# Optimization experiments

Hardware: AMD Instinct MI355X
Metric: run time of the kernel (lower is better)

## Reference

```python
import jax, jax.numpy as jnp
import numpy as np

NUM_USERS = 100000
NUM_ITEMS = 100000
EMB = 64
BATCH = 8192
TEMP = 0.2  # config['temperature']


def _l2norm(x):
    # F.normalize(x, dim=-1): x / max(||x||_2, eps)
    return x / jnp.maximum(jnp.linalg.norm(x, axis=-1, keepdims=True), 1e-12)


def setup_inputs() -> dict:
    key = jax.random.key(0)
    k1, k2, k3, k4, k5 = jax.random.split(key, 5)
    # xavier_uniform bounds for the embedding tables
    bu = float(np.sqrt(6.0 / (NUM_USERS + EMB)))
    bi = float(np.sqrt(6.0 / (NUM_ITEMS + EMB)))
    return {
        "user": jax.random.randint(k1, (BATCH,), 0, NUM_USERS),
        "positive": jax.random.randint(k2, (BATCH,), 0, NUM_ITEMS),
        "negative": jax.random.randint(k3, (BATCH,), 0, NUM_ITEMS),
        "user_emb_weight": jax.random.uniform(k4, (NUM_USERS, EMB), jnp.float32, -bu, bu),
        "item_emb_weight": jax.random.uniform(k5, (NUM_ITEMS, EMB), jnp.float32, -bi, bi),
    }


def reference(user, positive, negative, user_emb_weight, item_emb_weight):
    # encoder == 'MF': raw embedding tables are used directly.
    u = _l2norm(user_emb_weight[user])        # [B, D]
    p = _l2norm(item_emb_weight[positive])    # [B, D]

    # positive ('up') term: per-pair inner products
    ip = jnp.sum(u * p, axis=1)               # [B]
    up = jnp.mean(jnp.log(jnp.exp(ip / TEMP) + jnp.exp(ip * ip / TEMP)))

    # 'down' term. Original computes score over unique(user) x unique(positive)
    # weighted by the outer product of occurrence counts, then takes mean.
    # sum_{unique u,i} c_u*c_i*f(sim(u,i)) == sum over all BxB batch pairs of
    # f(sim(user_b, pos_b')), so we use the full batch cross product (jit-safe)
    # and divide by (#unique users * #unique items) for the mean.
    sim = u @ p.T                              # [B, B]
    score_sum = jnp.sum(jnp.exp(sim / TEMP) + jnp.exp(sim * sim / TEMP))
    nu = jnp.sum(jnp.bincount(user, length=NUM_USERS) > 0).astype(sim.dtype)
    ni = jnp.sum(jnp.bincount(positive, length=NUM_ITEMS) > 0).astype(sim.dtype)
    down = jnp.log(score_sum / (nu * ni))

    # loss_list = [-up, down]
    return jnp.stack([-up, down])
```

## Files before the change

kernel.cpp:

```cpp
#include <hip/hip_runtime.h>
#include <hip/hip_bf16.h>

#define EMB 64

typedef __attribute__((ext_vector_type(8))) short short8;
typedef __attribute__((ext_vector_type(8))) __bf16 bf16x8;
typedef __attribute__((ext_vector_type(4))) float f32x4;

__device__ inline f32x4 mfma16x16x32(short8 a, short8 b, f32x4 c) {
  return __builtin_amdgcn_mfma_f32_16x16x32_bf16(
      __builtin_bit_cast(bf16x8, a), __builtin_bit_cast(bf16x8, b), c, 0, 0, 0);
}

#define EXP2_HW __builtin_amdgcn_exp2f
#define C5LOG2E 7.213475204444817f

__global__ __launch_bounds__(256) void clear_kernel(uint4* __restrict__ p) {
  const int i = blockIdx.x * 256 + threadIdx.x;
  if (i < 12500) p[i] = make_uint4(0u, 0u, 0u, 0u);
}

__global__ __launch_bounds__(256) void prep_kernel(
    const int* __restrict__ user, const int* __restrict__ pos,
    const float* __restrict__ uw, const float* __restrict__ iw,
    __hip_bfloat16* __restrict__ u_bf, __hip_bfloat16* __restrict__ p_bf,
    unsigned char* __restrict__ uflag, unsigned char* __restrict__ iflag,
    float* __restrict__ up_p)
{
  const int tid  = threadIdx.x;
  const int wave = tid >> 6;
  const int lane = tid & 63;
  const int e    = lane & 15;
  const int row  = blockIdx.x * 16 + wave * 4 + (lane >> 4);

  const int uidx = user[row];
  const int pidx = pos[row];
  const float4 uv = *reinterpret_cast<const float4*>(&uw[(size_t)uidx * EMB + e * 4]);
  const float4 pv = *reinterpret_cast<const float4*>(&iw[(size_t)pidx * EMB + e * 4]);

  float us = uv.x*uv.x + uv.y*uv.y + uv.z*uv.z + uv.w*uv.w;
  float ps = pv.x*pv.x + pv.y*pv.y + pv.z*pv.z + pv.w*pv.w;
  #pragma unroll
  for (int off = 1; off < 16; off <<= 1) {
    us += __shfl_xor(us, off);
    ps += __shfl_xor(ps, off);
  }
  const float ur = 1.0f / fmaxf(sqrtf(us), 1e-12f);
  const float pr = 1.0f / fmaxf(sqrtf(ps), 1e-12f);
  const float4 un = make_float4(uv.x*ur, uv.y*ur, uv.z*ur, uv.w*ur);
  const float4 pn = make_float4(pv.x*pr, pv.y*pr, pv.z*pr, pv.w*pr);

  ushort4 ub, pb;
  ub.x = __bfloat16_as_ushort(__float2bfloat16(un.x));
  ub.y = __bfloat16_as_ushort(__float2bfloat16(un.y));
  ub.z = __bfloat16_as_ushort(__float2bfloat16(un.z));
  ub.w = __bfloat16_as_ushort(__float2bfloat16(un.w));
  pb.x = __bfloat16_as_ushort(__float2bfloat16(pn.x));
  pb.y = __bfloat16_as_ushort(__float2bfloat16(pn.y));
  pb.z = __bfloat16_as_ushort(__float2bfloat16(pn.z));
  pb.w = __bfloat16_as_ushort(__float2bfloat16(pn.w));
  *reinterpret_cast<ushort4*>(&u_bf[(size_t)row * EMB + e * 4]) = ub;
  *reinterpret_cast<ushort4*>(&p_bf[(size_t)row * EMB + e * 4]) = pb;

  float ip = un.x*pn.x + un.y*pn.y + un.z*pn.z + un.w*pn.w;
  #pragma unroll
  for (int off = 1; off < 16; off <<= 1) ip += __shfl_xor(ip, off);

  float upv = 0.0f;
  if (e == 0) {
    uflag[uidx] = 1;
    iflag[pidx] = 1;
    const float t = ip * C5LOG2E;
    upv = logf(EXP2_HW(t) + EXP2_HW(ip * t));
  }
  upv += __shfl_xor(upv, 16);
  upv += __shfl_xor(upv, 32);

  __shared__ float sred[4];
  if (lane == 0) sred[wave] = upv;
  __syncthreads();
  if (tid == 0)
    up_p[blockIdx.x] = (sred[0] + sred[1]) + (sred[2] + sred[3]);
}

__global__ __launch_bounds__(256) void gemm_kernel(
    const __hip_bfloat16* __restrict__ U, const __hip_bfloat16* __restrict__ P,
    float* __restrict__ dn_p)
{
  const int by  = blockIdx.x >> 4;
  const int bx0 = (blockIdx.x & 15) << 2;
  const int wave = threadIdx.x >> 6;
  const int lane = threadIdx.x & 63;
  const int r0 = by * 128 + (wave >> 1) * 64;
  const int lrow = lane & 15;
  const int lk   = (lane >> 4) * 8;

  short8 a[4][2];
  #pragma unroll
  for (int i = 0; i < 4; ++i)
    #pragma unroll
    for (int kk = 0; kk < 2; ++kk)
      a[i][kk] = *reinterpret_cast<const short8*>(
          &U[(size_t)(r0 + i * 16 + lrow) * EMB + kk * 32 + lk]);

  float s0 = 0.0f, s1 = 0.0f, s2 = 0.0f, s3 = 0.0f;

  auto loadB = [&](int t, int h, short8 (&b)[2][2]) {
    const int c0 = (bx0 + t) * 128 + (wave & 1) * 64 + h * 32;
    #pragma unroll
    for (int j = 0; j < 2; ++j)
      #pragma unroll
      for (int kk = 0; kk < 2; ++kk)
        b[j][kk] = *reinterpret_cast<const short8*>(
            &P[(size_t)(c0 + j * 16 + lrow) * EMB + kk * 32 + lk]);
  };
  auto procHalf = [&](const short8 (&b)[2][2]) {
    f32x4 acc[4][2] = {};
    #pragma unroll
    for (int i = 0; i < 4; ++i)
      #pragma unroll
      for (int j = 0; j < 2; ++j) {
        acc[i][j] = mfma16x16x32(a[i][0], b[j][0], acc[i][j]);
        acc[i][j] = mfma16x16x32(a[i][1], b[j][1], acc[i][j]);
      }
    #pragma unroll
    for (int i = 0; i < 4; ++i)
      #pragma unroll
      for (int j = 0; j < 2; ++j)
        #pragma unroll
        for (int r = 0; r < 4; ++r) {
          const float v  = acc[i][j][r];
          const float tt = v * C5LOG2E;
          if (j) { s2 += EXP2_HW(tt); s3 += EXP2_HW(v * tt); }
          else   { s0 += EXP2_HW(tt); s1 += EXP2_HW(v * tt); }
        }
  };

  short8 bA[2][2], bB[2][2];
  loadB(0, 0, bA);
  #pragma unroll 1
  for (int t = 0; t < 4; ++t) {
    loadB(t, 1, bB);
    procHalf(bA);
    loadB((t + 1) & 3, 0, bA);
    procHalf(bB);
  }

  float s = (s0 + s1) + (s2 + s3);
  #pragma unroll
  for (int off = 32; off; off >>= 1) s += __shfl_xor(s, off);

  __shared__ float sred[4];
  if (lane == 0) sred[wave] = s;
  __syncthreads();
  if (threadIdx.x == 0)
    dn_p[blockIdx.x] = (sred[0] + sred[1]) + (sred[2] + sred[3]);
}

__global__ __launch_bounds__(1024) void finalize_kernel(
    const float* __restrict__ up_p, const float* __restrict__ dn_p,
    const uint4* __restrict__ uflag4, const uint4* __restrict__ iflag4,
    float* __restrict__ out)
{
  const int tid  = threadIdx.x;
  const int wave = tid >> 6;
  const int lane = tid & 63;

  float upv = (tid < 512) ? up_p[tid] : 0.0f;
  float dnv = dn_p[tid];
  int uc = 0, ic = 0;
  for (int i = tid; i < 6250; i += 1024) {
    uint4 v = uflag4[i];
    uc += __popc(v.x) + __popc(v.y) + __popc(v.z) + __popc(v.w);
    uint4 w = iflag4[i];
    ic += __popc(w.x) + __popc(w.y) + __popc(w.z) + __popc(w.w);
  }

  #pragma unroll
  for (int off = 32; off; off >>= 1) {
    upv += __shfl_xor(upv, off);
    dnv += __shfl_xor(dnv, off);
    uc  += __shfl_xor(uc, off);
    ic  += __shfl_xor(ic, off);
  }

  __shared__ float sf[2][16];
  __shared__ int   si[2][16];
  if (lane == 0) { sf[0][wave] = upv; sf[1][wave] = dnv; si[0][wave] = uc; si[1][wave] = ic; }
  __syncthreads();
  if (tid == 0) {
    float usum = 0.0f, dsum = 0.0f; int nu = 0, ni = 0;
    #pragma unroll
    for (int w = 0; w < 16; ++w) {
      usum += sf[0][w]; dsum += sf[1][w]; nu += si[0][w]; ni += si[1][w];
    }
    out[0] = -(usum / 8192.0f);
    out[1] = logf(dsum / ((float)nu * (float)ni));
  }
}

extern "C" void kernel_launch(void* const* d_in, const int* in_sizes, int n_in,
                              void* d_out, int out_size, void* d_ws, size_t ws_size,
                              hipStream_t stream) {
  const int*   user = (const int*)d_in[0];
  const int*   pos  = (const int*)d_in[1];
  const float* uw   = (const float*)d_in[3];
  const float* iw   = (const float*)d_in[4];
  float* out = (float*)d_out;

  char* ws = (char*)d_ws;
  __hip_bfloat16* u_bf = (__hip_bfloat16*)(ws);
  __hip_bfloat16* p_bf = (__hip_bfloat16*)(ws + (1u << 20));
  uint4* flag4 = (uint4*)(ws + (2u << 20));
  unsigned char* uflag = (unsigned char*)flag4;
  unsigned char* iflag = uflag + 100000;
  float* up_p = (float*)(ws + (2u << 20) + 200704);
  float* dn_p = up_p + 512;

  clear_kernel<<<49, 256, 0, stream>>>(flag4);
  prep_kernel<<<512, 256, 0, stream>>>(user, pos, uw, iw, u_bf, p_bf,
                                       uflag, iflag, up_p);
  gemm_kernel<<<1024, 256, 0, stream>>>(u_bf, p_bf, dn_p);
  finalize_kernel<<<1, 1024, 0, stream>>>(up_p, dn_p,
                                          (const uint4*)uflag,
                                          (const uint4*)iflag, out);
}
```

Baseline: 42.56 us.

## Fuse finalize into GEMM via last-block counter and LDS bitmap unique count

Removes the clear kernel and the finalize kernel. The last GEMM block to finish, found through an atomic counter that prep_kernel resets, builds the unique-user and unique-item bitmaps in shared memory and performs the final reduction. This cuts two kernel launches and the global flag-array traffic. The cost is a 25KB shared bitmap in every GEMM block, which may reduce occupancy, plus the loss of the software double-buffering of B loads.

```diff
diff --git a/kernel.cpp b/kernel.cpp
--- a/kernel.cpp
+++ b/kernel.cpp
@@ -14,24 +14,20 @@
 
 #define EXP2_HW __builtin_amdgcn_exp2f
 #define C5LOG2E 7.213475204444817f
-
-__global__ __launch_bounds__(256) void clear_kernel(uint4* __restrict__ p) {
-  const int i = blockIdx.x * 256 + threadIdx.x;
-  if (i < 12500) p[i] = make_uint4(0u, 0u, 0u, 0u);
-}
 
 __global__ __launch_bounds__(256) void prep_kernel(
     const int* __restrict__ user, const int* __restrict__ pos,
     const float* __restrict__ uw, const float* __restrict__ iw,
     __hip_bfloat16* __restrict__ u_bf, __hip_bfloat16* __restrict__ p_bf,
-    unsigned char* __restrict__ uflag, unsigned char* __restrict__ iflag,
-    float* __restrict__ up_p)
+    float* __restrict__ up_p, unsigned int* __restrict__ done_cnt)
 {
   const int tid  = threadIdx.x;
   const int wave = tid >> 6;
   const int lane = tid & 63;
   const int e    = lane & 15;
   const int row  = blockIdx.x * 16 + wave * 4 + (lane >> 4);
+
+  if (blockIdx.x == 0 && tid == 0) *done_cnt = 0u;
 
   const int uidx = user[row];
   const int pidx = pos[row];
@@ -68,8 +64,6 @@
 
   float upv = 0.0f;
   if (e == 0) {
-    uflag[uidx] = 1;
-    iflag[pidx] = 1;
     const float t = ip * C5LOG2E;
     upv = logf(EXP2_HW(t) + EXP2_HW(ip * t));
   }
@@ -85,15 +79,22 @@
 
 __global__ __launch_bounds__(256) void gemm_kernel(
     const __hip_bfloat16* __restrict__ U, const __hip_bfloat16* __restrict__ P,
-    float* __restrict__ dn_p)
+    const int* __restrict__ user, const int* __restrict__ pos,
+    const float* __restrict__ up_p, float* __restrict__ dn_p,
+    unsigned int* __restrict__ done_cnt, float* __restrict__ out)
 {
-  const int by  = blockIdx.x >> 4;
-  const int bx0 = (blockIdx.x & 15) << 2;
-  const int wave = threadIdx.x >> 6;
-  const int lane = threadIdx.x & 63;
-  const int r0 = by * 128 + (wave >> 1) * 64;
+  const int tid  = threadIdx.x;
+  const int by   = blockIdx.x >> 4;
+  const int bx0  = (blockIdx.x & 15) << 2;
+  const int wave = tid >> 6;
+  const int lane = tid & 63;
+  const int r0   = by * 128 + (wave >> 1) * 64;
   const int lrow = lane & 15;
   const int lk   = (lane >> 4) * 8;
+
+  __shared__ float sredf[4];
+  __shared__ unsigned int bitmap[6250];
+  __shared__ unsigned int is_last;
 
   short8 a[4][2];
   #pragma unroll
@@ -105,16 +106,18 @@
 
   float s0 = 0.0f, s1 = 0.0f, s2 = 0.0f, s3 = 0.0f;
 
-  auto loadB = [&](int t, int h, short8 (&b)[2][2]) {
-    const int c0 = (bx0 + t) * 128 + (wave & 1) * 64 + h * 32;
+  #pragma unroll 1
+  for (int s = 0; s < 8; ++s) {
+    const int c0 = (bx0 + (s >> 1)) * 128 + (wave & 1) * 64 + (s & 1) * 32;
+
+    short8 b[2][2];
     #pragma unroll
     for (int j = 0; j < 2; ++j)
       #pragma unroll
       for (int kk = 0; kk < 2; ++kk)
         b[j][kk] = *reinterpret_cast<const short8*>(
             &P[(size_t)(c0 + j * 16 + lrow) * EMB + kk * 32 + lk]);
-  };
-  auto procHalf = [&](const short8 (&b)[2][2]) {
+
     f32x4 acc[4][2] = {};
     #pragma unroll
     for (int i = 0; i < 4; ++i)
@@ -123,6 +126,7 @@
         acc[i][j] = mfma16x16x32(a[i][0], b[j][0], acc[i][j]);
         acc[i][j] = mfma16x16x32(a[i][1], b[j][1], acc[i][j]);
       }
+
     #pragma unroll
     for (int i = 0; i < 4; ++i)
       #pragma unroll
@@ -134,47 +138,42 @@
           if (j) { s2 += EXP2_HW(tt); s3 += EXP2_HW(v * tt); }
           else   { s0 += EXP2_HW(tt); s1 += EXP2_HW(v * tt); }
         }
-  };
-
-  short8 bA[2][2], bB[2][2];
-  loadB(0, 0, bA);
-  #pragma unroll 1
-  for (int t = 0; t < 4; ++t) {
-    loadB(t, 1, bB);
-    procHalf(bA);
-    loadB((t + 1) & 3, 0, bA);
-    procHalf(bB);
   }
 
   float s = (s0 + s1) + (s2 + s3);
   #pragma unroll
   for (int off = 32; off; off >>= 1) s += __shfl_xor(s, off);
 
-  __shared__ float sred[4];
-  if (lane == 0) sred[wave] = s;
-  __syncthreads();
-  if (threadIdx.x == 0)
-    dn_p[blockIdx.x] = (sred[0] + sred[1]) + (sred[2] + sred[3]);
-}
-
-__global__ __launch_bounds__(1024) void finalize_kernel(
-    const float* __restrict__ up_p, const float* __restrict__ dn_p,
-    const uint4* __restrict__ uflag4, const uint4* __restrict__ iflag4,
-    float* __restrict__ out)
-{
-  const int tid  = threadIdx.x;
-  const int wave = tid >> 6;
-  const int lane = tid & 63;
-
-  float upv = (tid < 512) ? up_p[tid] : 0.0f;
-  float dnv = dn_p[tid];
+  if (lane == 0) sredf[wave] = s;
+  __syncthreads();
+  if (tid == 0)
+    dn_p[blockIdx.x] = (sredf[0] + sredf[1]) + (sredf[2] + sredf[3]);
+
+  __threadfence();
+  if (tid == 0)
+    is_last = (atomicAdd(done_cnt, 1u) == 1023u) ? 1u : 0u;
+  __syncthreads();
+  if (!is_last) return;
+  __threadfence();
+
+  for (int i = tid; i < 6250; i += 256) bitmap[i] = 0u;
+  __syncthreads();
+  for (int i = tid; i < 8192; i += 256) {
+    const int u = user[i];
+    const int p = pos[i];
+    atomicOr(&bitmap[u >> 5], 1u << (u & 31));
+    atomicOr(&bitmap[3125 + (p >> 5)], 1u << (p & 31));
+  }
+  __syncthreads();
+
   int uc = 0, ic = 0;
-  for (int i = tid; i < 6250; i += 1024) {
-    uint4 v = uflag4[i];
-    uc += __popc(v.x) + __popc(v.y) + __popc(v.z) + __popc(v.w);
-    uint4 w = iflag4[i];
-    ic += __popc(w.x) + __popc(w.y) + __popc(w.z) + __popc(w.w);
-  }
+  for (int i = tid; i < 3125; i += 256) {
+    uc += __popc(bitmap[i]);
+    ic += __popc(bitmap[3125 + i]);
+  }
+  float upv = 0.0f, dnv = 0.0f;
+  for (int i = tid; i < 512; i += 256)  upv += up_p[i];
+  for (int i = tid; i < 1024; i += 256) dnv += dn_p[i];
 
   #pragma unroll
   for (int off = 32; off; off >>= 1) {
@@ -184,16 +183,15 @@
     ic  += __shfl_xor(ic, off);
   }
 
-  __shared__ float sf[2][16];
-  __shared__ int   si[2][16];
-  if (lane == 0) { sf[0][wave] = upv; sf[1][wave] = dnv; si[0][wave] = uc; si[1][wave] = ic; }
+  __shared__ float ff[2][4];
+  __shared__ int   gg[2][4];
+  if (lane == 0) { ff[0][wave] = upv; ff[1][wave] = dnv; gg[0][wave] = uc; gg[1][wave] = ic; }
   __syncthreads();
   if (tid == 0) {
-    float usum = 0.0f, dsum = 0.0f; int nu = 0, ni = 0;
-    #pragma unroll
-    for (int w = 0; w < 16; ++w) {
-      usum += sf[0][w]; dsum += sf[1][w]; nu += si[0][w]; ni += si[1][w];
-    }
+    const float usum = (ff[0][0] + ff[0][1]) + (ff[0][2] + ff[0][3]);
+    const float dsum = (ff[1][0] + ff[1][1]) + (ff[1][2] + ff[1][3]);
+    const int   nu   = gg[0][0] + gg[0][1] + gg[0][2] + gg[0][3];
+    const int   ni   = gg[1][0] + gg[1][1] + gg[1][2] + gg[1][3];
     out[0] = -(usum / 8192.0f);
     out[1] = logf(dsum / ((float)nu * (float)ni));
   }
@@ -211,17 +209,12 @@
   char* ws = (char*)d_ws;
   __hip_bfloat16* u_bf = (__hip_bfloat16*)(ws);
   __hip_bfloat16* p_bf = (__hip_bfloat16*)(ws + (1u << 20));
-  uint4* flag4 = (uint4*)(ws + (2u << 20));
-  unsigned char* uflag = (unsigned char*)flag4;
-  unsigned char* iflag = uflag + 100000;
-  float* up_p = (float*)(ws + (2u << 20) + 200704);
+  float* up_p = (float*)(ws + (2u << 20));
   float* dn_p = up_p + 512;
-
-  clear_kernel<<<49, 256, 0, stream>>>(flag4);
+  unsigned int* done_cnt = (unsigned int*)(dn_p + 1024);
+
   prep_kernel<<<512, 256, 0, stream>>>(user, pos, uw, iw, u_bf, p_bf,
-                                       uflag, iflag, up_p);
-  gemm_kernel<<<1024, 256, 0, stream>>>(u_bf, p_bf, dn_p);
-  finalize_kernel<<<1, 1024, 0, stream>>>(up_p, dn_p,
-                                          (const uint4*)uflag,
-                                          (const uint4*)iflag, out);
-}
+                                       up_p, done_cnt);
+  gemm_kernel<<<1024, 256, 0, stream>>>(u_bf, p_bf, user, pos,
+                                        up_p, dn_p, done_cnt, out);
+}
```

Measured after the change: 112.1 us. +163.5%, slower.
